# Kernel tuning notes

Measured on AMD Instinct MI355X. Metric: run time of the kernel, lower is better.

## Reference

```python
import jax, jax.numpy as jnp
import numpy as np

SEQ, BZ, DIM = 2048, 16, 1024
NUM_LANG, DICT_LEN = 16, 32000


def setup_inputs() -> dict:
    key = jax.random.key(0)
    ks = jax.random.split(key, 6)
    x = jax.random.normal(ks[0], (SEQ, BZ, DIM), dtype=jnp.float32)
    # raw language ids live at the tail of the dictionary: dict_len-1-raw in [0, num_lang)
    raw = DICT_LEN - 1 - jax.random.randint(ks[1], (BZ,), 0, NUM_LANG)
    W_base = jax.random.normal(ks[2], (DIM, DIM), dtype=jnp.float32) * (DIM ** -0.5)
    b_base = jax.random.normal(ks[3], (DIM,), dtype=jnp.float32) * 0.02
    W = jax.random.uniform(ks[4], (NUM_LANG, DIM, DIM), dtype=jnp.float32) * (DIM ** -0.5)
    bias = jax.random.uniform(ks[5], (NUM_LANG, DIM), dtype=jnp.float32)
    return {"x": x, "lang_ids": raw, "W_base": W_base, "b_base": b_base,
            "W": W, "bias": bias, "dict_len": DICT_LEN, "num_lang": NUM_LANG}


def reference(x, lang_ids, W_base, b_base, W, bias, dict_len, num_lang):
    # Map raw ids to expert indices in [0, num_lang)
    ids = dict_len - 1 - lang_ids                      # [bz]
    # base_model (nn.Linear): h = x @ W_base.T + b_base
    h = jnp.einsum('sbd,ed->sbe', x, W_base) + b_base  # [seq, bz, dim]
    # The original pads each language group to max group size, runs a batched
    # einsum 'abcd,ade->abce' over languages, then scatters back with per-lang
    # bias. Mathematically each batch column j gets W[lang_j] applied:
    We = W[ids]                                        # [bz, dim, dim]
    out = jnp.einsum('sbd,bde->sbe', h, We) + bias[ids][None, :, :]
    return out
```

## Files before the change

kernel.cpp:

```cpp
#include <hip/hip_runtime.h>
#include <stdint.h>

typedef unsigned short u16;
typedef unsigned int u32;
typedef __bf16 bf16x8 __attribute__((ext_vector_type(8)));
typedef float f32x4 __attribute__((ext_vector_type(4)));
typedef float f32x16 __attribute__((ext_vector_type(16)));

#define SEQ 2048
#define BZ 16
#define DIM 1024

__device__ __forceinline__ u16 f2bf(float f) {
    union { float f; u32 u; } a; a.f = f;
    u32 r = a.u + 0x7FFFu + ((a.u >> 16) & 1u);
    return (u16)(r >> 16);
}
__device__ __forceinline__ float bf2f(u16 u) {
    union { u32 u; float f; } a; a.u = ((u32)u) << 16;
    return a.f;
}
__device__ __forceinline__ void async16(const u16* g, u16* l) {
    __builtin_amdgcn_global_load_lds(
        (const __attribute__((address_space(1))) void*)g,
        (__attribute__((address_space(3))) void*)l, 16, 0, 0);
}

__global__ void convert_x(const float* __restrict__ x, u16* __restrict__ xb)
{
    int s = blockIdx.x;
    int t = threadIdx.x;
    const float4* src = (const float4*)(x + (size_t)s * BZ * DIM);
    #pragma unroll
    for (int j = 0; j < 16; j++) {
        int idx = j * 256 + t;
        float4 v = src[idx];
        int e = idx * 4;
        int b = e >> 10, d = e & 1023;
        u32 lo = f2bf(v.x) | ((u32)f2bf(v.y) << 16);
        u32 hi = f2bf(v.z) | ((u32)f2bf(v.w) << 16);
        *(uint2*)(xb + ((size_t)b * SEQ + s) * DIM + d) = make_uint2(lo, hi);
    }
}

__global__ void transpose_cvt(const float* __restrict__ W,
                              const float* __restrict__ W_base,
                              const int* __restrict__ lang_ids,
                              const int* __restrict__ dict_len,
                              u16* __restrict__ Wt,
                              u16* __restrict__ Wbt)
{
    int z = blockIdx.z;
    const float* S;
    u16* D;
    if (z < BZ) {
        int id = dict_len[0] - 1 - lang_ids[z];
        S = W + (size_t)id * DIM * DIM;
        D = Wbt + (size_t)z * DIM * DIM;
    } else {
        S = W_base;
        D = Wt;
    }
    __shared__ float tile[32][33];
    int tx = threadIdx.x, ty = threadIdx.y;
    int x0 = blockIdx.x * 32, y0 = blockIdx.y * 32;
    #pragma unroll
    for (int i = 0; i < 4; i++)
        tile[ty + 8 * i][tx] = S[(size_t)(y0 + ty + 8 * i) * DIM + x0 + tx];
    __syncthreads();
    #pragma unroll
    for (int i = 0; i < 4; i++)
        D[(size_t)(x0 + ty + 8 * i) * DIM + y0 + tx] = f2bf(tile[tx][ty + 8 * i]);
}

__global__ void bb_kernel(const u16* __restrict__ Wbt,
                          const float* __restrict__ b_base,
                          const float* __restrict__ bias,
                          const int* __restrict__ lang_ids,
                          const int* __restrict__ dict_len,
                          float* __restrict__ bb)
{
    int gw = blockIdx.x * 4 + (threadIdx.x >> 6);
    int b = gw >> 10;
    int f = gw & 1023;
    int lane = threadIdx.x & 63;
    const u16* row = Wbt + ((size_t)b * DIM + f) * DIM;
    float s = 0.f;
    #pragma unroll
    for (int i = 0; i < DIM / 64; i++)
        s += bf2f(row[lane + 64 * i]) * b_base[lane + 64 * i];
    #pragma unroll
    for (int off = 32; off; off >>= 1)
        s += __shfl_xor(s, off, 64);
    if (lane == 0) {
        int id = dict_len[0] - 1 - lang_ids[b];
        bb[b * DIM + f] = s + bias[(size_t)id * DIM + f];
    }
}


#define RD_A(m, kk, l) (((m)*32 + ((l) & 31)) * 32 + ((((kk)*2 + ((l) >> 5)) ^ ((l) & 3)) * 8))
#define RD_B(w, n, kk, l) (((w)*64 + (n)*32 + ((l) & 31)) * 32 + ((((kk)*2 + ((l) >> 5)) ^ ((l) & 3)) * 8))

__global__ __launch_bounds__(256, 2)
void gemm1_kernel(const u16* __restrict__ Wbt,
                  const u16* __restrict__ Wt,
                  u16* __restrict__ CT)
{
    int bid = blockIdx.x;
    int virt = ((bid & 7) << 6) + (bid >> 3);
    int b    = virt >> 5;
    int rem  = virt & 31;
    int m0   = (rem >> 2) << 7;
    int n0   = (rem & 3) << 8;

    const u16* A = Wbt + (size_t)b * DIM * DIM;
    const u16* B = Wt;
    u16* C = CT + (size_t)b * DIM * DIM;

    __shared__ u16 As[2 * 128 * 32];
    __shared__ u16 Bs[2 * 256 * 32];

    int tid = threadIdx.x;
    int w = tid >> 6, l = tid & 63;
    int lr = l & 31, h = l >> 5;

    int srow = l >> 2;
    int chunk = (l & 3) ^ (srow & 3);
    const u16* gA[2]; const u16* gB[4];
    int lA[2], lB[4];
    #pragma unroll
    for (int j = 0; j < 2; j++) {
        int row = w * 32 + j * 16 + srow;
        gA[j] = A + (size_t)(m0 + row) * DIM + chunk * 8;
        lA[j] = (w * 32 + j * 16) * 32;
    }
    #pragma unroll
    for (int j = 0; j < 4; j++) {
        int row = w * 64 + j * 16 + srow;
        gB[j] = B + (size_t)(n0 + row) * DIM + chunk * 8;
        lB[j] = (w * 64 + j * 16) * 32;
    }

    f32x16 acc[4][2];
    #pragma unroll
    for (int m = 0; m < 4; m++)
        #pragma unroll
        for (int n = 0; n < 2; n++)
            #pragma unroll
            for (int e = 0; e < 16; e++) acc[m][n][e] = 0.f;

    #pragma unroll
    for (int j = 0; j < 2; j++) async16(gA[j], As + lA[j]);
    #pragma unroll
    for (int j = 0; j < 4; j++) async16(gB[j], Bs + lB[j]);
    #pragma unroll
    for (int j = 0; j < 2; j++) gA[j] += 32;
    #pragma unroll
    for (int j = 0; j < 4; j++) gB[j] += 32;
    __syncthreads();

    int cur = 0;
    for (int t = 0; t < DIM / 32; t++) {
        if (t + 1 < DIM / 32) {
            int ao = (cur ^ 1) * 4096, bo = (cur ^ 1) * 8192;
            #pragma unroll
            for (int j = 0; j < 2; j++) { async16(gA[j], As + ao + lA[j]); gA[j] += 32; }
            #pragma unroll
            for (int j = 0; j < 4; j++) { async16(gB[j], Bs + bo + lB[j]); gB[j] += 32; }
        }
        const u16* ra = As + cur * 4096;
        const u16* rb = Bs + cur * 8192;
        bf16x8 af[4][2], bfv[2][2];
        #pragma unroll
        for (int m = 0; m < 4; m++)
            #pragma unroll
            for (int kk = 0; kk < 2; kk++)
                af[m][kk] = *(const bf16x8*)&ra[RD_A(m, kk, l)];
        #pragma unroll
        for (int n = 0; n < 2; n++)
            #pragma unroll
            for (int kk = 0; kk < 2; kk++)
                bfv[n][kk] = *(const bf16x8*)&rb[RD_B(w, n, kk, l)];
        #pragma unroll
        for (int kk = 0; kk < 2; kk++)
            #pragma unroll
            for (int m = 0; m < 4; m++)
                #pragma unroll
                for (int n = 0; n < 2; n++)
                    acc[m][n] = __builtin_amdgcn_mfma_f32_32x32x16_bf16(
                        af[m][kk], bfv[n][kk], acc[m][n], 0, 0, 0);
        __syncthreads();
        cur ^= 1;
    }

    #pragma unroll
    for (int m = 0; m < 4; m++)
        #pragma unroll
        for (int n = 0; n < 2; n++) {
            int col = n0 + w * 64 + n * 32 + lr;
            #pragma unroll
            for (int reg = 0; reg < 16; reg++) {
                int row = m0 + m * 32 + (reg & 3) + 8 * (reg >> 2) + 4 * h;
                C[(size_t)row * DIM + col] = f2bf(acc[m][n][reg]);
            }
        }
}

__global__ __launch_bounds__(256, 2)
void gemm2_kernel(const u16* __restrict__ xb,
                  const u16* __restrict__ CT,
                  const float* __restrict__ bb,
                  float* __restrict__ out)
{
    int bid = blockIdx.x;
    int virt = ((bid & 7) << 7) + (bid >> 3);
    int b    = virt >> 6;
    int rem  = virt & 63;
    int s0   = (rem >> 2) << 7;
    int f0   = (rem & 3) << 8;

    const u16* A  = xb + (size_t)b * SEQ * DIM;
    const u16* Bm = CT + (size_t)b * DIM * DIM;

    __shared__ u16 As[2 * 128 * 32];
    __shared__ u16 Bs[2 * 256 * 32];

    int tid = threadIdx.x;
    int w = tid >> 6, l = tid & 63;
    int lr = l & 31, h = l >> 5;

    int srow = l >> 2;
    int chunk = (l & 3) ^ (srow & 3);
    const u16* gA[2]; const u16* gB[4];
    int lA[2], lB[4];
    #pragma unroll
    for (int j = 0; j < 2; j++) {
        int row = w * 32 + j * 16 + srow;
        gA[j] = A + (size_t)(s0 + row) * DIM + chunk * 8;
        lA[j] = (w * 32 + j * 16) * 32;
    }
    #pragma unroll
    for (int j = 0; j < 4; j++) {
        int row = w * 64 + j * 16 + srow;
        gB[j] = Bm + (size_t)(f0 + row) * DIM + chunk * 8;
        lB[j] = (w * 64 + j * 16) * 32;
    }

    f32x16 acc[4][2];
    #pragma unroll
    for (int m = 0; m < 4; m++)
        #pragma unroll
        for (int n = 0; n < 2; n++)
            #pragma unroll
            for (int e = 0; e < 16; e++) acc[m][n][e] = 0.f;

    #pragma unroll
    for (int j = 0; j < 2; j++) async16(gA[j], As + lA[j]);
    #pragma unroll
    for (int j = 0; j < 4; j++) async16(gB[j], Bs + lB[j]);
    #pragma unroll
    for (int j = 0; j < 2; j++) gA[j] += 32;
    #pragma unroll
    for (int j = 0; j < 4; j++) gB[j] += 32;
    __syncthreads();

    int cur = 0;
    for (int t = 0; t < DIM / 32; t++) {
        if (t + 1 < DIM / 32) {
            int ao = (cur ^ 1) * 4096, bo = (cur ^ 1) * 8192;
            #pragma unroll
            for (int j = 0; j < 2; j++) { async16(gA[j], As + ao + lA[j]); gA[j] += 32; }
            #pragma unroll
            for (int j = 0; j < 4; j++) { async16(gB[j], Bs + bo + lB[j]); gB[j] += 32; }
        }
        const u16* ra = As + cur * 4096;
        const u16* rb = Bs + cur * 8192;
        bf16x8 af[4][2], bfv[2][2];
        #pragma unroll
        for (int m = 0; m < 4; m++)
            #pragma unroll
            for (int kk = 0; kk < 2; kk++)
                af[m][kk] = *(const bf16x8*)&ra[RD_A(m, kk, l)];
        #pragma unroll
        for (int n = 0; n < 2; n++)
            #pragma unroll
            for (int kk = 0; kk < 2; kk++)
                bfv[n][kk] = *(const bf16x8*)&rb[RD_B(w, n, kk, l)];
        #pragma unroll
        for (int kk = 0; kk < 2; kk++)
            #pragma unroll
            for (int m = 0; m < 4; m++)
                #pragma unroll
                for (int n = 0; n < 2; n++)
                    acc[m][n] = __builtin_amdgcn_mfma_f32_32x32x16_bf16(
                        af[m][kk], bfv[n][kk], acc[m][n], 0, 0, 0);
        __syncthreads();
        cur ^= 1;
    }

    #pragma unroll
    for (int n = 0; n < 2; n++) {
        int col = f0 + w * 64 + n * 32 + lr;
        float bv = bb[b * DIM + col];
        #pragma unroll
        for (int m = 0; m < 4; m++)
            #pragma unroll
            for (int reg = 0; reg < 16; reg++) {
                int row = s0 + m * 32 + (reg & 3) + 8 * (reg >> 2) + 4 * h;
                out[((size_t)row * BZ + b) * DIM + col] = acc[m][n][reg] + bv;
            }
    }
}

extern "C" void kernel_launch(void* const* d_in, const int* in_sizes, int n_in,
                              void* d_out, int out_size, void* d_ws, size_t ws_size,
                              hipStream_t stream)
{
    const float* x        = (const float*)d_in[0];
    const int*   lang_ids = (const int*)d_in[1];
    const float* W_base   = (const float*)d_in[2];
    const float* b_base   = (const float*)d_in[3];
    const float* W        = (const float*)d_in[4];
    const float* bias     = (const float*)d_in[5];
    const int*   dict_len = (const int*)d_in[6];
    float* out = (float*)d_out;

    char* ws = (char*)d_ws;
    u16*  Wt  = (u16*)ws;
    u16*  Wbt = (u16*)(ws + (size_t)(2u << 20));
    u16*  CT  = (u16*)(ws + (size_t)(34u << 20));
    float* bb = (float*)(ws + (size_t)(66u << 20));
    u16*  xb  = (u16*)(ws + (size_t)(67u << 20));

    convert_x<<<dim3(SEQ, 1, 1), 256, 0, stream>>>(x, xb);
    transpose_cvt<<<dim3(32, 32, 17), dim3(32, 8, 1), 0, stream>>>(
        W, W_base, lang_ids, dict_len, Wt, Wbt);
    bb_kernel<<<dim3(4096, 1, 1), 256, 0, stream>>>(
        Wbt, b_base, bias, lang_ids, dict_len, bb);
    gemm1_kernel<<<dim3(512, 1, 1), 256, 0, stream>>>(Wbt, Wt, CT);
    gemm2_kernel<<<dim3(1024, 1, 1), 256, 0, stream>>>(xb, CT, bb, out);
}
```

Measured before the change: 441.7 us.

## Switch GEMMs to 16x16x32 MFMA, drop LDS swizzle, fuse prep kernels

Both GEMM kernels move from 32x32x16 MFMA tiles to 16x16x32 tiles, with a new fragment layout and epilogue. The XOR swizzle on LDS chunk placement is removed, so reads now use a plain row-major index. The x conversion and weight transpose kernels are merged into one launch to save a launch. Dropping the swizzle risks LDS bank conflicts on the 16-byte fragment reads, and the smaller MFMA shape issues more instructions per tile.

```diff
diff --git a/kernel.cpp b/kernel.cpp
--- a/kernel.cpp
+++ b/kernel.cpp
@@ -5,7 +5,6 @@
 typedef unsigned int u32;
 typedef __bf16 bf16x8 __attribute__((ext_vector_type(8)));
 typedef float f32x4 __attribute__((ext_vector_type(4)));
-typedef float f32x16 __attribute__((ext_vector_type(16)));
 
 #define SEQ 2048
 #define BZ 16
@@ -26,31 +25,36 @@
         (__attribute__((address_space(3))) void*)l, 16, 0, 0);
 }
 
-__global__ void convert_x(const float* __restrict__ x, u16* __restrict__ xb)
-{
-    int s = blockIdx.x;
+__global__ void prep_kernel(const float* __restrict__ x,
+                            const float* __restrict__ W,
+                            const float* __restrict__ W_base,
+                            const int* __restrict__ lang_ids,
+                            const int* __restrict__ dict_len,
+                            u16* __restrict__ xb,
+                            u16* __restrict__ Wt,
+                            u16* __restrict__ Wbt)
+{
+    int bid = blockIdx.x;
     int t = threadIdx.x;
-    const float4* src = (const float4*)(x + (size_t)s * BZ * DIM);
-    #pragma unroll
-    for (int j = 0; j < 16; j++) {
-        int idx = j * 256 + t;
-        float4 v = src[idx];
-        int e = idx * 4;
-        int b = e >> 10, d = e & 1023;
-        u32 lo = f2bf(v.x) | ((u32)f2bf(v.y) << 16);
-        u32 hi = f2bf(v.z) | ((u32)f2bf(v.w) << 16);
-        *(uint2*)(xb + ((size_t)b * SEQ + s) * DIM + d) = make_uint2(lo, hi);
-    }
-}
-
-__global__ void transpose_cvt(const float* __restrict__ W,
-                              const float* __restrict__ W_base,
-                              const int* __restrict__ lang_ids,
-                              const int* __restrict__ dict_len,
-                              u16* __restrict__ Wt,
-                              u16* __restrict__ Wbt)
-{
-    int z = blockIdx.z;
+    if (bid < SEQ) {
+        int s = bid;
+        const float4* src = (const float4*)(x + (size_t)s * BZ * DIM);
+        #pragma unroll
+        for (int j = 0; j < 16; j++) {
+            int idx = j * 256 + t;
+            float4 v = src[idx];
+            int e = idx * 4;
+            int b = e >> 10, d = e & 1023;
+            u32 lo = f2bf(v.x) | ((u32)f2bf(v.y) << 16);
+            u32 hi = f2bf(v.z) | ((u32)f2bf(v.w) << 16);
+            *(uint2*)(xb + ((size_t)b * SEQ + s) * DIM + d) = make_uint2(lo, hi);
+        }
+        return;
+    }
+    int tid2 = bid - SEQ;
+    int z = tid2 >> 10;
+    int yx = tid2 & 1023;
+    int by = yx >> 5, bx = yx & 31;
     const float* S;
     u16* D;
     if (z < BZ) {
@@ -62,8 +66,8 @@
         D = Wt;
     }
     __shared__ float tile[32][33];
-    int tx = threadIdx.x, ty = threadIdx.y;
-    int x0 = blockIdx.x * 32, y0 = blockIdx.y * 32;
+    int tx = t & 31, ty = t >> 5;
+    int x0 = bx * 32, y0 = by * 32;
     #pragma unroll
     for (int i = 0; i < 4; i++)
         tile[ty + 8 * i][tx] = S[(size_t)(y0 + ty + 8 * i) * DIM + x0 + tx];
@@ -99,9 +103,6 @@
 }
 
 
-#define RD_A(m, kk, l) (((m)*32 + ((l) & 31)) * 32 + ((((kk)*2 + ((l) >> 5)) ^ ((l) & 3)) * 8))
-#define RD_B(w, n, kk, l) (((w)*64 + (n)*32 + ((l) & 31)) * 32 + ((((kk)*2 + ((l) >> 5)) ^ ((l) & 3)) * 8))
-
 __global__ __launch_bounds__(256, 2)
 void gemm1_kernel(const u16* __restrict__ Wbt,
                   const u16* __restrict__ Wt,
@@ -123,10 +124,10 @@
 
     int tid = threadIdx.x;
     int w = tid >> 6, l = tid & 63;
-    int lr = l & 31, h = l >> 5;
+    int lr = l & 15, quad = l >> 4;
 
     int srow = l >> 2;
-    int chunk = (l & 3) ^ (srow & 3);
+    int chunk = l & 3;
     const u16* gA[2]; const u16* gB[4];
     int lA[2], lB[4];
     #pragma unroll
@@ -142,13 +143,13 @@
         lB[j] = (w * 64 + j * 16) * 32;
     }
 
-    f32x16 acc[4][2];
-    #pragma unroll
-    for (int m = 0; m < 4; m++)
-        #pragma unroll
-        for (int n = 0; n < 2; n++)
-            #pragma unroll
-            for (int e = 0; e < 16; e++) acc[m][n][e] = 0.f;
+    f32x4 acc[8][4];
+    #pragma unroll
+    for (int m = 0; m < 8; m++)
+        #pragma unroll
+        for (int n = 0; n < 4; n++)
+            #pragma unroll
+            for (int e = 0; e < 4; e++) acc[m][n][e] = 0.f;
 
     #pragma unroll
     for (int j = 0; j < 2; j++) async16(gA[j], As + lA[j]);
@@ -171,40 +172,33 @@
         }
         const u16* ra = As + cur * 4096;
         const u16* rb = Bs + cur * 8192;
-        bf16x8 af[4][2], bfv[2][2];
-        #pragma unroll
-        for (int m = 0; m < 4; m++)
-            #pragma unroll
-            for (int kk = 0; kk < 2; kk++)
-                af[m][kk] = *(const bf16x8*)&ra[RD_A(m, kk, l)];
-        #pragma unroll
-        for (int n = 0; n < 2; n++)
-            #pragma unroll
-            for (int kk = 0; kk < 2; kk++)
-                bfv[n][kk] = *(const bf16x8*)&rb[RD_B(w, n, kk, l)];
-        #pragma unroll
-        for (int kk = 0; kk < 2; kk++)
-            #pragma unroll
-            for (int m = 0; m < 4; m++)
-                #pragma unroll
-                for (int n = 0; n < 2; n++)
-                    acc[m][n] = __builtin_amdgcn_mfma_f32_32x32x16_bf16(
-                        af[m][kk], bfv[n][kk], acc[m][n], 0, 0, 0);
+        bf16x8 af[8], bfv[4];
+        #pragma unroll
+        for (int m = 0; m < 8; m++)
+            af[m] = *(const bf16x8*)&ra[(m * 16 + lr) * 32 + quad * 8];
+        #pragma unroll
+        for (int n = 0; n < 4; n++)
+            bfv[n] = *(const bf16x8*)&rb[(w * 64 + n * 16 + lr) * 32 + quad * 8];
+        #pragma unroll
+        for (int m = 0; m < 8; m++)
+            #pragma unroll
+            for (int n = 0; n < 4; n++)
+                acc[m][n] = __builtin_amdgcn_mfma_f32_16x16x32_bf16(
+                    af[m], bfv[n], acc[m][n], 0, 0, 0);
         __syncthreads();
         cur ^= 1;
     }
-
-    #pragma unroll
-    for (int m = 0; m < 4; m++)
-        #pragma unroll
-        for (int n = 0; n < 2; n++) {
-            int col = n0 + w * 64 + n * 32 + lr;
-            #pragma unroll
-            for (int reg = 0; reg < 16; reg++) {
-                int row = m0 + m * 32 + (reg & 3) + 8 * (reg >> 2) + 4 * h;
-                C[(size_t)row * DIM + col] = f2bf(acc[m][n][reg]);
-            }
-        }
+    #pragma unroll
+    for (int m = 0; m < 8; m++) {
+        int fr = m0 + m * 16 + quad * 4;
+        #pragma unroll
+        for (int n = 0; n < 4; n++) {
+            int dc = n0 + w * 64 + n * 16 + lr;
+            #pragma unroll
+            for (int rr = 0; rr < 4; rr++)
+                C[(size_t)(fr + rr) * DIM + dc] = f2bf(acc[m][n][rr]);
+        }
+    }
 }
 
 __global__ __launch_bounds__(256, 2)
@@ -228,10 +222,10 @@
 
     int tid = threadIdx.x;
     int w = tid >> 6, l = tid & 63;
-    int lr = l & 31, h = l >> 5;
+    int lr = l & 15, quad = l >> 4;
 
     int srow = l >> 2;
-    int chunk = (l & 3) ^ (srow & 3);
+    int chunk = l & 3;
     const u16* gA[2]; const u16* gB[4];
     int lA[2], lB[4];
     #pragma unroll
@@ -247,13 +241,13 @@
         lB[j] = (w * 64 + j * 16) * 32;
     }
 
-    f32x16 acc[4][2];
-    #pragma unroll
-    for (int m = 0; m < 4; m++)
-        #pragma unroll
-        for (int n = 0; n < 2; n++)
-            #pragma unroll
-            for (int e = 0; e < 16; e++) acc[m][n][e] = 0.f;
+    f32x4 acc[8][4];
+    #pragma unroll
+    for (int m = 0; m < 8; m++)
+        #pragma unroll
+        for (int n = 0; n < 4; n++)
+            #pragma unroll
+            for (int e = 0; e < 4; e++) acc[m][n][e] = 0.f;
 
     #pragma unroll
     for (int j = 0; j < 2; j++) async16(gA[j], As + lA[j]);
@@ -276,40 +270,34 @@
         }
         const u16* ra = As + cur * 4096;
         const u16* rb = Bs + cur * 8192;
-        bf16x8 af[4][2], bfv[2][2];
-        #pragma unroll
-        for (int m = 0; m < 4; m++)
-            #pragma unroll
-            for (int kk = 0; kk < 2; kk++)
-                af[m][kk] = *(const bf16x8*)&ra[RD_A(m, kk, l)];
-        #pragma unroll
-        for (int n = 0; n < 2; n++)
-            #pragma unroll
-            for (int kk = 0; kk < 2; kk++)
-                bfv[n][kk] = *(const bf16x8*)&rb[RD_B(w, n, kk, l)];
-        #pragma unroll
-        for (int kk = 0; kk < 2; kk++)
-            #pragma unroll
-            for (int m = 0; m < 4; m++)
-                #pragma unroll
-                for (int n = 0; n < 2; n++)
-                    acc[m][n] = __builtin_amdgcn_mfma_f32_32x32x16_bf16(
-                        af[m][kk], bfv[n][kk], acc[m][n], 0, 0, 0);
+        bf16x8 af[8], bfv[4];
+        #pragma unroll
+        for (int m = 0; m < 8; m++)
+            af[m] = *(const bf16x8*)&ra[(m * 16 + lr) * 32 + quad * 8];
+        #pragma unroll
+        for (int n = 0; n < 4; n++)
+            bfv[n] = *(const bf16x8*)&rb[(w * 64 + n * 16 + lr) * 32 + quad * 8];
+        #pragma unroll
+        for (int m = 0; m < 8; m++)
+            #pragma unroll
+            for (int n = 0; n < 4; n++)
+                acc[m][n] = __builtin_amdgcn_mfma_f32_16x16x32_bf16(
+                    af[m], bfv[n], acc[m][n], 0, 0, 0);
         __syncthreads();
         cur ^= 1;
     }
 
     #pragma unroll
-    for (int n = 0; n < 2; n++) {
-        int col = f0 + w * 64 + n * 32 + lr;
+    for (int n = 0; n < 4; n++) {
+        int col = f0 + w * 64 + n * 16 + lr;
         float bv = bb[b * DIM + col];
         #pragma unroll
-        for (int m = 0; m < 4; m++)
-            #pragma unroll
-            for (int reg = 0; reg < 16; reg++) {
-                int row = s0 + m * 32 + (reg & 3) + 8 * (reg >> 2) + 4 * h;
-                out[((size_t)row * BZ + b) * DIM + col] = acc[m][n][reg] + bv;
-            }
+        for (int m = 0; m < 8; m++) {
+            int sr = s0 + m * 16 + quad * 4;
+            #pragma unroll
+            for (int rr = 0; rr < 4; rr++)
+                out[((size_t)(sr + rr) * BZ + b) * DIM + col] = acc[m][n][rr] + bv;
+        }
     }
 }
 
@@ -333,9 +321,8 @@
     float* bb = (float*)(ws + (size_t)(66u << 20));
     u16*  xb  = (u16*)(ws + (size_t)(67u << 20));
 
-    convert_x<<<dim3(SEQ, 1, 1), 256, 0, stream>>>(x, xb);
-    transpose_cvt<<<dim3(32, 32, 17), dim3(32, 8, 1), 0, stream>>>(
-        W, W_base, lang_ids, dict_len, Wt, Wbt);
+    prep_kernel<<<dim3(SEQ + 17 * 1024, 1, 1), 256, 0, stream>>>(
+        x, W, W_base, lang_ids, dict_len, xb, Wt, Wbt);
     bb_kernel<<<dim3(4096, 1, 1), 256, 0, stream>>>(
         Wbt, b_base, bias, lang_ids, dict_len, bb);
     gemm1_kernel<<<dim3(512, 1, 1), 256, 0, stream>>>(Wbt, Wt, CT);
```

New measurement: 430.7 us. 2.5% less time.
